# Performance work log

Measured on AMD Instinct MI355X. Metric: run time of the kernel, lower is better.

The kernel has to match this reference:

```python
import jax, jax.numpy as jnp
import numpy as np

N_EMBED = 1024
HEAD_SIZE = 128
B, T = 4, 2048

def setup_inputs() -> dict:
    key = jax.random.key(0)
    kx, kq, kk, kv = jax.random.split(key, 4)
    bound = 1.0 / np.sqrt(N_EMBED)  # torch Linear default init range
    x = jax.random.normal(kx, (B, T, N_EMBED), dtype=jnp.float32)
    Wq = jax.random.uniform(kq, (N_EMBED, HEAD_SIZE), jnp.float32, -bound, bound)
    Wk = jax.random.uniform(kk, (N_EMBED, HEAD_SIZE), jnp.float32, -bound, bound)
    Wv = jax.random.uniform(kv, (N_EMBED, HEAD_SIZE), jnp.float32, -bound, bound)
    return {"x": x, "Wq": Wq, "Wk": Wk, "Wv": Wv}

def reference(x, Wq, Wk, Wv):
    Bn, Tn, C = x.shape
    q = x @ Wq  # [B,T,H]
    k = x @ Wk
    v = x @ Wv
    # NOTE: original scales by C**-0.5 where C = n_embed (not head_size)
    scale = C ** (-0.5)
    wei = jnp.einsum('bqh,bkh->bqk', q, k) * scale  # [B,T,T]
    causal = jnp.tril(jnp.ones((Tn, Tn), dtype=bool))
    wei = jnp.where(causal, wei, -jnp.inf)
    wei = jax.nn.softmax(wei, axis=-1)
    # dropout p=0.0 -> identity
    return jnp.einsum('bqk,bkh->bqh', wei, v)
```

## Files before the change

kernel.cpp:

```cpp
#include <hip/hip_runtime.h>
#include <stdint.h>

#define B_ 4
#define T_ 2048
#define C_ 1024
#define H_ 128
#define NEG_BIG -3.0e38f

typedef __attribute__((ext_vector_type(8))) short short8;
typedef __attribute__((ext_vector_type(4))) float f32x4;
typedef __attribute__((ext_vector_type(4))) unsigned short ushort4v;
typedef __attribute__((ext_vector_type(8))) unsigned short ushort8v;

__device__ __forceinline__ unsigned short f2bf(float f) {
  union { float f; unsigned u; } cv; cv.f = f;
  return (unsigned short)((cv.u + 0x8000u) >> 16);
}

__device__ __forceinline__ float bf2f(unsigned short s) {
  union { unsigned u; float f; } cv; cv.u = ((unsigned)s) << 16;
  return cv.f;
}

__device__ __forceinline__ void gld16(const void* g, void* l) {
  __builtin_amdgcn_global_load_lds(
      (const __attribute__((address_space(1))) unsigned int*)g,
      (__attribute__((address_space(3))) unsigned int*)l, 16, 0, 0);
}

#define CSCALE 0.045084220027780106f

__global__ __launch_bounds__(256) void prep(const float* __restrict__ x,
                                            const float* __restrict__ Wq,
                                            const float* __restrict__ Wk,
                                            const float* __restrict__ Wv,
                                            unsigned short* __restrict__ xb,
                                            unsigned short* __restrict__ WbT) {
  if (blockIdx.x < 8192) {
    const int base = (blockIdx.x * 256 + threadIdx.x) * 4;
    f32x4 v = *(const f32x4*)(x + base);
    ushort4v p;
    p[0] = f2bf(v[0]); p[1] = f2bf(v[1]); p[2] = f2bf(v[2]); p[3] = f2bf(v[3]);
    *(ushort4v*)(xb + base) = p;
  } else {
    const int i = (blockIdx.x - 8192) * 256 + threadIdx.x;
    const int linear = i * 4;
    const int j = linear >> 10;
    const int k0 = linear & 1023;
    const float* W = (j < 128) ? Wq : (j < 256) ? Wk : Wv;
    const int h = j & 127;
    ushort4v p;
    p[0] = f2bf(W[(k0 + 0) * 128 + h]);
    p[1] = f2bf(W[(k0 + 1) * 128 + h]);
    p[2] = f2bf(W[(k0 + 2) * 128 + h]);
    p[3] = f2bf(W[(k0 + 3) * 128 + h]);
    *(ushort4v*)(WbT + linear) = p;
  }
}

__global__ __launch_bounds__(256) void qkv_proj(const unsigned short* __restrict__ xb,
                                                const unsigned short* __restrict__ WbT,
                                                unsigned short* __restrict__ Qb,
                                                unsigned short* __restrict__ Kb,
                                                unsigned short* __restrict__ VT) {
  __shared__ unsigned short As[2][128 * 64];
  __shared__ unsigned short Bs[2][96 * 64];

  const int tid  = threadIdx.x;
  const int wave = tid >> 6, lane = tid & 63;
  const int quad = lane >> 4, l15 = lane & 15;
  const int rb = blockIdx.x >> 2, cb = blockIdx.x & 3;
  const int gm0 = rb * 128, gn0 = cb * 96;
  const int wm = wave >> 1, wn = wave & 1;

  const int srow = lane >> 3, sslot = lane & 7;

  int aoff[4][2], boff[3][2];
#pragma unroll
  for (int mt = 0; mt < 4; ++mt) {
    const int r = wm * 64 + mt * 16 + l15;
#pragma unroll
    for (int ks = 0; ks < 2; ++ks)
      aoff[mt][ks] = r * 64 + (((ks * 4 + quad) ^ r) & 7) * 8;
  }
#pragma unroll
  for (int nt = 0; nt < 3; ++nt) {
    const int r = wn * 48 + nt * 16 + l15;
#pragma unroll
    for (int ks = 0; ks < 2; ++ks)
      boff[nt][ks] = r * 64 + (((ks * 4 + quad) ^ r) & 7) * 8;
  }

  f32x4 acc[4][3];
  const f32x4 zero4 = {0.f, 0.f, 0.f, 0.f};
#pragma unroll
  for (int mt = 0; mt < 4; ++mt)
#pragma unroll
    for (int nt = 0; nt < 3; ++nt) acc[mt][nt] = zero4;

#define STAGE_QKV(buf, kb_)                                                        \
  {                                                                                \
    const int ko = (kb_) * 64;                                                     \
    _Pragma("unroll")                                                              \
    for (int q = 0; q < 4; ++q) {                                                  \
      const int row = q * 32 + wave * 8 + srow;                                    \
      gld16(xb + (size_t)(gm0 + row) * C_ + ko + ((sslot ^ row) & 7) * 8,          \
            &As[buf][(q * 32 + wave * 8) * 64]);                                   \
    }                                                                              \
    _Pragma("unroll")                                                              \
    for (int q = 0; q < 3; ++q) {                                                  \
      const int row = wave * 24 + q * 8 + srow;                                    \
      gld16(WbT + (size_t)(gn0 + row) * C_ + ko + ((sslot ^ row) & 7) * 8,         \
            &Bs[buf][(wave * 24 + q * 8) * 64]);                                   \
    }                                                                              \
  }

  STAGE_QKV(0, 0);

  for (int kb = 0; kb < 16; ++kb) {
    __syncthreads();
    if (kb + 1 < 16) STAGE_QKV((kb + 1) & 1, kb + 1);
    const unsigned short* Ac = As[kb & 1];
    const unsigned short* Bc = Bs[kb & 1];
#pragma unroll
    for (int ks = 0; ks < 2; ++ks) {
      short8 b0 = *(const short8*)(Bc + boff[0][ks]);
      short8 b1 = *(const short8*)(Bc + boff[1][ks]);
      short8 b2 = *(const short8*)(Bc + boff[2][ks]);
#pragma unroll
      for (int mt = 0; mt < 4; ++mt) {
        short8 a = *(const short8*)(Ac + aoff[mt][ks]);
        acc[mt][0] = __builtin_amdgcn_mfma_f32_16x16x32_bf16(a, b0, acc[mt][0], 0, 0, 0);
        acc[mt][1] = __builtin_amdgcn_mfma_f32_16x16x32_bf16(a, b1, acc[mt][1], 0, 0, 0);
        acc[mt][2] = __builtin_amdgcn_mfma_f32_16x16x32_bf16(a, b2, acc[mt][2], 0, 0, 0);
      }
    }
  }
#undef STAGE_QKV

#pragma unroll
  for (int mt = 0; mt < 4; ++mt) {
    const int row0 = gm0 + wm * 64 + mt * 16 + quad * 4;
#pragma unroll
    for (int nt = 0; nt < 3; ++nt) {
      const int colbase = gn0 + wn * 48 + nt * 16;
      const int col = colbase + l15;
      if (colbase < 128) {
#pragma unroll
        for (int r = 0; r < 4; ++r)
          Qb[(size_t)(row0 + r) * H_ + col] = f2bf(acc[mt][nt][r] * CSCALE);
      } else if (colbase < 256) {
#pragma unroll
        for (int r = 0; r < 4; ++r)
          Kb[(size_t)(row0 + r) * H_ + (col - 128)] = f2bf(acc[mt][nt][r]);
      } else {
        const int h = col - 256;
        const int bidx = row0 >> 11;
        const int t0 = row0 & 2047;
        ushort4v pk;
        pk[0] = f2bf(acc[mt][nt][0]); pk[1] = f2bf(acc[mt][nt][1]);
        pk[2] = f2bf(acc[mt][nt][2]); pk[3] = f2bf(acc[mt][nt][3]);
        *(ushort4v*)(VT + (size_t)(bidx * H_ + h) * T_ + t0) = pk;
      }
    }
  }
}

__global__ __launch_bounds__(256, 2) void attn1(const unsigned short* __restrict__ Qb,
                                                const unsigned short* __restrict__ Kb,
                                                const unsigned short* __restrict__ VT,
                                                unsigned short* __restrict__ Opart,
                                                float* __restrict__ mpart,
                                                float* __restrict__ lpart,
                                                float* __restrict__ out) {
  __shared__ unsigned short Ks[2][64 * 128];
  __shared__ unsigned short Vs[2][128 * 64];
  __shared__ unsigned short Pls[4][16 * 72];
  __shared__ float Als[4][16];

  const int bid = blockIdx.x;
  const int b  = bid & 3;
  const int j  = (bid >> 2) & 31;
  const int ch = bid >> 7;
  if (ch * 8 > j) return;
  const int ntiles = min(8, j + 1 - ch * 8);

  const int tid  = threadIdx.x;
  const int wave = tid >> 6, lane = tid & 63;
  const int quad = lane >> 4, l15 = lane & 15;

  const unsigned short* qrow = Qb + (size_t)(b * T_ + j * 64 + wave * 16 + l15) * H_;
  short8 aq[4];
#pragma unroll
  for (int ks = 0; ks < 4; ++ks)
    aq[ks] = *(const short8*)(qrow + ks * 32 + quad * 8);

  const unsigned short* Kb_b = Kb + (size_t)(b * T_) * H_;
  const unsigned short* VT_b = VT + (size_t)(b * H_) * T_;

  const int k_row4 = lane >> 4, k_slot = lane & 15;
  const int v_row8 = lane >> 3, v_slot = lane & 7;

#define STAGE_KV(buf, kv0_)                                                        \
  {                                                                                \
    _Pragma("unroll")                                                              \
    for (int i = 0; i < 4; ++i) {                                                  \
      const int r = wave * 16 + i * 4 + k_row4;                                    \
      const int c2 = (k_slot & 8) | ((k_slot ^ r) & 7);                            \
      gld16(Kb_b + (size_t)((kv0_) + r) * H_ + c2 * 8,                             \
            &Ks[buf][(wave * 16 + i * 4) * 128]);                                  \
    }                                                                              \
    _Pragma("unroll")                                                              \
    for (int i = 0; i < 4; ++i) {                                                  \
      const int h = wave * 32 + i * 8 + v_row8;                                    \
      gld16(VT_b + (size_t)h * T_ + (kv0_) + ((v_slot ^ h) & 7) * 8,               \
            &Vs[buf][(wave * 32 + i * 8) * 64]);                                   \
    }                                                                              \
  }

  STAGE_KV(0, ch * 512);

  const f32x4 zero4 = {0.f, 0.f, 0.f, 0.f};
  f32x4 O[8];
#pragma unroll
  for (int nth = 0; nth < 8; ++nth) O[nth] = zero4;
  float m_ = NEG_BIG, l_ = 0.f;

  for (int t = 0; t < ntiles; ++t) {
    __syncthreads();
    const int kv0 = ch * 512 + t * 64;
    if (t + 1 < ntiles) STAGE_KV((t + 1) & 1, kv0 + 64);

    const unsigned short* kb = Ks[t & 1];
    f32x4 ST[4];
    ST[0] = zero4; ST[1] = zero4; ST[2] = zero4; ST[3] = zero4;
#pragma unroll
    for (int ntl = 0; ntl < 4; ++ntl) {
      const int kvr = ntl * 16 + l15;
#pragma unroll
      for (int ks = 0; ks < 4; ++ks) {
        const int c = ks * 4 + quad;
        const int slot = (c & 8) | ((c ^ kvr) & 7);
        short8 kf = *(const short8*)(kb + kvr * 128 + slot * 8);
        ST[ntl] = __builtin_amdgcn_mfma_f32_16x16x32_bf16(kf, aq[ks], ST[ntl], 0, 0, 0);
      }
    }

    if (ch * 8 + t == j) {
      const int ql = j * 64 + wave * 16 + l15;
#pragma unroll
      for (int ntl = 0; ntl < 4; ++ntl)
#pragma unroll
        for (int r = 0; r < 4; ++r) {
          const int kl = kv0 + ntl * 16 + quad * 4 + r;
          if (kl > ql) ST[ntl][r] = NEG_BIG;
        }
    }

    float vmax = ST[0][0];
#pragma unroll
    for (int ntl = 0; ntl < 4; ++ntl)
#pragma unroll
      for (int r = 0; r < 4; ++r) vmax = fmaxf(vmax, ST[ntl][r]);
    vmax = fmaxf(vmax, __shfl_xor(vmax, 16));
    vmax = fmaxf(vmax, __shfl_xor(vmax, 32));
    const float mn = fmaxf(m_, vmax);
    const float alpha = __builtin_amdgcn_exp2f(m_ - mn);
    m_ = mn;
    float s = 0.f;
#pragma unroll
    for (int ntl = 0; ntl < 4; ++ntl)
#pragma unroll
      for (int r = 0; r < 4; ++r) {
        const float p = __builtin_amdgcn_exp2f(ST[ntl][r] - mn);
        ST[ntl][r] = p;
        s += p;
      }
    s += __shfl_xor(s, 16);
    s += __shfl_xor(s, 32);
    l_ = l_ * alpha + s;

#pragma unroll
    for (int ntl = 0; ntl < 4; ++ntl) {
      ushort4v pk;
      pk[0] = f2bf(ST[ntl][0]); pk[1] = f2bf(ST[ntl][1]);
      pk[2] = f2bf(ST[ntl][2]); pk[3] = f2bf(ST[ntl][3]);
      *(ushort4v*)(&Pls[wave][l15 * 72 + ntl * 16 + quad * 4]) = pk;
    }

    if (lane < 16) Als[wave][lane] = alpha;
    if (!__all(alpha == 1.f)) {
      f32x4 al4 = *(const f32x4*)&Als[wave][quad * 4];
#pragma unroll
      for (int nth = 0; nth < 8; ++nth)
#pragma unroll
        for (int r = 0; r < 4; ++r) O[nth][r] *= al4[r];
    }

    const unsigned short* vb = Vs[t & 1];
    short8 ap0 = *(const short8*)(&Pls[wave][l15 * 72 + quad * 8]);
    short8 ap1 = *(const short8*)(&Pls[wave][l15 * 72 + 32 + quad * 8]);
#pragma unroll
    for (int nth = 0; nth < 8; ++nth) {
      const int h = nth * 16 + l15;
      short8 v0 = *(const short8*)(vb + h * 64 + ((quad ^ h) & 7) * 8);
      short8 v1 = *(const short8*)(vb + h * 64 + (((4 + quad) ^ h) & 7) * 8);
      O[nth] = __builtin_amdgcn_mfma_f32_16x16x32_bf16(ap0, v0, O[nth], 0, 0, 0);
      O[nth] = __builtin_amdgcn_mfma_f32_16x16x32_bf16(ap1, v1, O[nth], 0, 0, 0);
    }
  }
#undef STAGE_KV

  if ((j >> 3) == 0) {
    if (lane < 16) Als[wave][lane] = 1.0f / l_;
    f32x4 li4 = *(const f32x4*)&Als[wave][quad * 4];
    float* op = out + (size_t)(b * T_ + j * 64 + wave * 16) * H_;
#pragma unroll
    for (int nth = 0; nth < 8; ++nth)
#pragma unroll
      for (int r = 0; r < 4; ++r)
        op[(quad * 4 + r) * H_ + nth * 16 + l15] = O[nth][r] * li4[r];
  } else {
    const int pid = (b * 32 + j) * 4 + ch;
    unsigned short* po = Opart + (size_t)(pid * 64 + wave * 16) * H_;
#pragma unroll
    for (int nth = 0; nth < 8; ++nth)
#pragma unroll
      for (int r = 0; r < 4; ++r)
        po[(quad * 4 + r) * H_ + nth * 16 + l15] = f2bf(O[nth][r]);
    if (lane < 16) {
      mpart[pid * 64 + wave * 16 + lane] = m_;
      lpart[pid * 64 + wave * 16 + lane] = l_;
    }
  }
}

__global__ __launch_bounds__(256) void attn2(const unsigned short* __restrict__ Opart,
                                             const float* __restrict__ mpart,
                                             const float* __restrict__ lpart,
                                             float* __restrict__ out) {
  const int b = blockIdx.x & 3;
  const int j = 8 + (blockIdx.x >> 2);
  const int nch = (j >> 3) + 1;
  const int tid = threadIdx.x;
  const int qh = tid >> 4;
  const int h0 = (tid & 15) * 8;
  const int pbase = (b * 32 + j) * 4;

#pragma unroll
  for (int i = 0; i < 4; ++i) {
    const int q = qh + i * 16;
    float m_fin = NEG_BIG;
    for (int ch = 0; ch < nch; ++ch)
      m_fin = fmaxf(m_fin, mpart[(pbase + ch) * 64 + q]);
    float lf = 0.f;
    float o[8];
#pragma unroll
    for (int c = 0; c < 8; ++c) o[c] = 0.f;
    for (int ch = 0; ch < nch; ++ch) {
      const int pid = pbase + ch;
      const float sc = __builtin_amdgcn_exp2f(mpart[pid * 64 + q] - m_fin);
      lf += sc * lpart[pid * 64 + q];
      ushort8v pv = *(const ushort8v*)(Opart + (size_t)(pid * 64 + q) * H_ + h0);
#pragma unroll
      for (int c = 0; c < 8; ++c) o[c] += sc * bf2f(pv[c]);
    }
    const float inv = 1.0f / lf;
    float* op = out + (size_t)(b * T_ + j * 64 + q) * H_ + h0;
    f32x4 v0 = {o[0] * inv, o[1] * inv, o[2] * inv, o[3] * inv};
    f32x4 v1 = {o[4] * inv, o[5] * inv, o[6] * inv, o[7] * inv};
    *(f32x4*)(op) = v0;
    *(f32x4*)(op + 4) = v1;
  }
}

extern "C" void kernel_launch(void* const* d_in, const int* in_sizes, int n_in,
                              void* d_out, int out_size, void* d_ws, size_t ws_size,
                              hipStream_t stream) {
  const float* x  = (const float*)d_in[0];
  const float* Wq = (const float*)d_in[1];
  const float* Wk = (const float*)d_in[2];
  const float* Wv = (const float*)d_in[3];
  float* out = (float*)d_out;

  char* ws = (char*)d_ws;
  unsigned short* xb  = (unsigned short*)(ws);
  unsigned short* WbT = (unsigned short*)(ws + 16777216);
  unsigned short* Qb  = (unsigned short*)(ws + 17563648);
  unsigned short* Kb  = (unsigned short*)(ws + 19660800);
  unsigned short* VT  = (unsigned short*)(ws + 21757952);
  unsigned short* Opart = (unsigned short*)(ws);
  float* mpart = (float*)(ws + 8388608);
  float* lpart = (float*)(ws + 8519680);

  prep<<<dim3(8576), dim3(256), 0, stream>>>(x, Wq, Wk, Wv, xb, WbT);
  qkv_proj<<<dim3(256), dim3(256), 0, stream>>>(xb, WbT, Qb, Kb, VT);
  attn1<<<dim3(512), dim3(256), 0, stream>>>(Qb, Kb, VT, Opart, mpart, lpart, out);
  attn2<<<dim3(96), dim3(256), 0, stream>>>(Opart, mpart, lpart, out);
}
```

Baseline: 137.2 us.

## Fuse fp32-to-bf16 conversion of x into QKV projection loads

The separate prep pass that converted the whole fp32 input to a bf16 buffer is removed. The projection kernel now loads fp32 x straight into registers, converts it, and writes the bf16 tile into swizzled LDS one stage ahead, after the MFMA work. Only the weight transpose remains as a small prep kernel. This drops a 32MB read plus 16MB write-and-reread round trip and one launch. In exchange, the A-tile staging becomes register-mediated, which uses more VGPRs and the LDS writes happen synchronously. The projection kernel also reads x twice as much data, since it now loads fp32 instead of bf16.

```diff
diff --git a/kernel.cpp b/kernel.cpp
--- a/kernel.cpp
+++ b/kernel.cpp
@@ -30,35 +30,25 @@
 
 #define CSCALE 0.045084220027780106f
 
-__global__ __launch_bounds__(256) void prep(const float* __restrict__ x,
-                                            const float* __restrict__ Wq,
-                                            const float* __restrict__ Wk,
-                                            const float* __restrict__ Wv,
-                                            unsigned short* __restrict__ xb,
-                                            unsigned short* __restrict__ WbT) {
-  if (blockIdx.x < 8192) {
-    const int base = (blockIdx.x * 256 + threadIdx.x) * 4;
-    f32x4 v = *(const f32x4*)(x + base);
-    ushort4v p;
-    p[0] = f2bf(v[0]); p[1] = f2bf(v[1]); p[2] = f2bf(v[2]); p[3] = f2bf(v[3]);
-    *(ushort4v*)(xb + base) = p;
-  } else {
-    const int i = (blockIdx.x - 8192) * 256 + threadIdx.x;
-    const int linear = i * 4;
-    const int j = linear >> 10;
-    const int k0 = linear & 1023;
-    const float* W = (j < 128) ? Wq : (j < 256) ? Wk : Wv;
-    const int h = j & 127;
-    ushort4v p;
-    p[0] = f2bf(W[(k0 + 0) * 128 + h]);
-    p[1] = f2bf(W[(k0 + 1) * 128 + h]);
-    p[2] = f2bf(W[(k0 + 2) * 128 + h]);
-    p[3] = f2bf(W[(k0 + 3) * 128 + h]);
-    *(ushort4v*)(WbT + linear) = p;
-  }
-}
-
-__global__ __launch_bounds__(256) void qkv_proj(const unsigned short* __restrict__ xb,
+__global__ __launch_bounds__(256) void prep_w(const float* __restrict__ Wq,
+                                              const float* __restrict__ Wk,
+                                              const float* __restrict__ Wv,
+                                              unsigned short* __restrict__ WbT) {
+  const int i = blockIdx.x * 256 + threadIdx.x;
+  const int linear = i * 4;
+  const int j = linear >> 10;
+  const int k0 = linear & 1023;
+  const float* W = (j < 128) ? Wq : (j < 256) ? Wk : Wv;
+  const int h = j & 127;
+  ushort4v p;
+  p[0] = f2bf(W[(k0 + 0) * 128 + h]);
+  p[1] = f2bf(W[(k0 + 1) * 128 + h]);
+  p[2] = f2bf(W[(k0 + 2) * 128 + h]);
+  p[3] = f2bf(W[(k0 + 3) * 128 + h]);
+  *(ushort4v*)(WbT + linear) = p;
+}
+
+__global__ __launch_bounds__(256) void qkv_proj(const float* __restrict__ x,
                                                 const unsigned short* __restrict__ WbT,
                                                 unsigned short* __restrict__ Qb,
                                                 unsigned short* __restrict__ Kb,
@@ -74,6 +64,8 @@
   const int wm = wave >> 1, wn = wave & 1;
 
   const int srow = lane >> 3, sslot = lane & 7;
+  const int axr = tid >> 3, axc = tid & 7;
+  const float* gAx = x + (size_t)(gm0 + axr) * C_ + axc * 8;
 
   int aoff[4][2], boff[3][2];
 #pragma unroll
@@ -98,15 +90,9 @@
 #pragma unroll
     for (int nt = 0; nt < 3; ++nt) acc[mt][nt] = zero4;
 
-#define STAGE_QKV(buf, kb_)                                                        \
+#define STAGE_B(buf, kb_)                                                          \
   {                                                                                \
     const int ko = (kb_) * 64;                                                     \
-    _Pragma("unroll")                                                              \
-    for (int q = 0; q < 4; ++q) {                                                  \
-      const int row = q * 32 + wave * 8 + srow;                                    \
-      gld16(xb + (size_t)(gm0 + row) * C_ + ko + ((sslot ^ row) & 7) * 8,          \
-            &As[buf][(q * 32 + wave * 8) * 64]);                                   \
-    }                                                                              \
     _Pragma("unroll")                                                              \
     for (int q = 0; q < 3; ++q) {                                                  \
       const int row = wave * 24 + q * 8 + srow;                                    \
@@ -115,13 +101,40 @@
     }                                                                              \
   }
 
-  STAGE_QKV(0, 0);
+#define LOAD_A(ko_)                                                                \
+  _Pragma("unroll")                                                                \
+  for (int q = 0; q < 4; ++q) {                                                    \
+    av0[q] = *(const f32x4*)(gAx + (size_t)(q * 32) * C_ + (ko_));                 \
+    av1[q] = *(const f32x4*)(gAx + (size_t)(q * 32) * C_ + (ko_) + 4);             \
+  }
+
+#define WRITE_A(buf)                                                               \
+  _Pragma("unroll")                                                                \
+  for (int q = 0; q < 4; ++q) {                                                    \
+    const int row = axr + q * 32;                                                  \
+    short8 aw;                                                                     \
+    _Pragma("unroll")                                                              \
+    for (int e = 0; e < 4; ++e) {                                                  \
+      aw[e]     = (short)f2bf(av0[q][e]);                                          \
+      aw[4 + e] = (short)f2bf(av1[q][e]);                                          \
+    }                                                                              \
+    *(short8*)(&As[buf][row * 64 + ((axc ^ row) & 7) * 8]) = aw;                   \
+  }
+
+  f32x4 av0[4], av1[4];
+  LOAD_A(0);
+  STAGE_B(0, 0);
+  WRITE_A(0);
 
   for (int kb = 0; kb < 16; ++kb) {
     __syncthreads();
-    if (kb + 1 < 16) STAGE_QKV((kb + 1) & 1, kb + 1);
-    const unsigned short* Ac = As[kb & 1];
-    const unsigned short* Bc = Bs[kb & 1];
+    const int cur = kb & 1, nxt = cur ^ 1;
+    if (kb + 1 < 16) {
+      LOAD_A((kb + 1) * 64);
+      STAGE_B(nxt, kb + 1);
+    }
+    const unsigned short* Ac = As[cur];
+    const unsigned short* Bc = Bs[cur];
 #pragma unroll
     for (int ks = 0; ks < 2; ++ks) {
       short8 b0 = *(const short8*)(Bc + boff[0][ks]);
@@ -135,8 +148,11 @@
         acc[mt][2] = __builtin_amdgcn_mfma_f32_16x16x32_bf16(a, b2, acc[mt][2], 0, 0, 0);
       }
     }
-  }
-#undef STAGE_QKV
+    if (kb + 1 < 16) WRITE_A(nxt);
+  }
+#undef STAGE_B
+#undef LOAD_A
+#undef WRITE_A
 
 #pragma unroll
   for (int mt = 0; mt < 4; ++mt) {
@@ -384,17 +400,16 @@
   float* out = (float*)d_out;
 
   char* ws = (char*)d_ws;
-  unsigned short* xb  = (unsigned short*)(ws);
-  unsigned short* WbT = (unsigned short*)(ws + 16777216);
-  unsigned short* Qb  = (unsigned short*)(ws + 17563648);
-  unsigned short* Kb  = (unsigned short*)(ws + 19660800);
-  unsigned short* VT  = (unsigned short*)(ws + 21757952);
-  unsigned short* Opart = (unsigned short*)(ws);
-  float* mpart = (float*)(ws + 8388608);
-  float* lpart = (float*)(ws + 8519680);
-
-  prep<<<dim3(8576), dim3(256), 0, stream>>>(x, Wq, Wk, Wv, xb, WbT);
-  qkv_proj<<<dim3(256), dim3(256), 0, stream>>>(xb, WbT, Qb, Kb, VT);
+  unsigned short* WbT = (unsigned short*)(ws);
+  unsigned short* Qb  = (unsigned short*)(ws + 1048576);
+  unsigned short* Kb  = (unsigned short*)(ws + 3145728);
+  unsigned short* VT  = (unsigned short*)(ws + 5242880);
+  unsigned short* Opart = (unsigned short*)(ws + 8388608);
+  float* mpart = (float*)(ws + 16777216);
+  float* lpart = (float*)(ws + 16908288);
+
+  prep_w<<<dim3(384), dim3(256), 0, stream>>>(Wq, Wk, Wv, WbT);
+  qkv_proj<<<dim3(256), dim3(256), 0, stream>>>(x, WbT, Qb, Kb, VT);
   attn1<<<dim3(512), dim3(256), 0, stream>>>(Qb, Kb, VT, Opart, mpart, lpart, out);
   attn2<<<dim3(96), dim3(256), 0, stream>>>(Opart, mpart, lpart, out);
 }
```

New measurement: 136.5 us. No clear change (-0.5%).
